# Kernel optimization log

Measured on AMD Instinct MI355X. Metric: run time of the kernel, lower is better.

Reference implementation:

```python
import jax, jax.numpy as jnp
import numpy as np

# physical system constants (from source)
M1, M2 = 1.0, 1.5
K1, K2 = 2.0, 3.0
C1, C2 = 0.5, 0.8
KARNOPP_DV = 0.01
REF_AMP, REF_OMEGA = 0.5, 0.5  # x2_ref_func(t) = 0.5*sin(0.5*t)

N = 1 << 20   # batch of states
H = 64        # friction_nn hidden dim


def setup_inputs() -> dict:
    key = jax.random.key(0)
    ks = jax.random.split(key, 8)
    return {
        "t": jax.random.uniform(ks[0], (N,), dtype=jnp.float32) * 10.0,
        "z": jax.random.normal(ks[1], (5, N), dtype=jnp.float32),
        "logK": jax.random.normal(ks[2], (), dtype=jnp.float32) * 0.1,
        "logz": jax.random.normal(ks[3], (), dtype=jnp.float32) * 0.1 - 0.5,
        "logp": jax.random.normal(ks[4], (), dtype=jnp.float32) * 0.1 + 0.5,
        "W1": jax.random.normal(ks[5], (1, H), dtype=jnp.float32) * 0.5,
        "b1": jnp.zeros((H,), dtype=jnp.float32),
        "W2": jax.random.normal(ks[6], (H, 2), dtype=jnp.float32) * 0.5,
        "b2": jnp.zeros((2,), dtype=jnp.float32),
    }


def _friction_nn(v2, W1, b1, W2, b2):
    # tiny MLP: 1 -> H -> 2, softplus heads for positive magnitudes
    h = jnp.tanh(v2[:, None] * W1[0] + b1)          # [N, H]
    out = h @ W2 + b2                                # [N, 2]
    kinetic_mag = jax.nn.softplus(out[:, 0])
    stiction_limit = jax.nn.softplus(out[:, 1])
    return kinetic_mag, stiction_limit


def reference(t, z, logK, logz, logp, W1, b1, W2, b2):
    x1, v1, x2, v2, xc = z
    K = jnp.exp(logK)
    z_ctrl = jnp.exp(logz)
    p_ctrl = jnp.exp(logp)

    x2_ref = REF_AMP * jnp.sin(REF_OMEGA * t)
    e = x2_ref - x2
    d_xc = -p_ctrl * xc + e
    u = K * (z_ctrl - p_ctrl) * xc + K * e

    dx1_dt = v1
    dv1_dt = (u - K1 * x1 - C1 * v1 - K2 * (x1 - x2) - C2 * (v1 - v2)) / M1
    dx2_dt = v2

    F_net = K2 * (x1 - x2) + C2 * (v1 - v2)
    kinetic_mag, stiction_limit = _friction_nn(v2, W1, b1, W2, b2)
    is_static = jnp.abs(v2) < KARNOPP_DV
    F_static = -jnp.clip(F_net, -stiction_limit, stiction_limit)
    F_kinetic = -kinetic_mag * jnp.sign(v2)
    F_friction = jnp.where(is_static, F_static, F_kinetic)
    dv2_dt = (F_net + F_friction) / M2

    return jnp.stack([dx1_dt, dv1_dt, dx2_dt, dv2_dt, d_xc])  # [5, N]
```

## Files before the change

kernel.cpp:

```cpp
#include <hip/hip_runtime.h>
#include <hip/hip_bf16.h>

#define M1_C 1.0f
#define M2_INV (1.0f / 1.5f)
#define K1_C 2.0f
#define K2_C 3.0f
#define C1_C 0.5f
#define C2_C 0.8f
#define KARNOPP_DV 0.01f
#define REF_AMP 0.5f
#define REF_OMEGA 0.5f
#define HDIM 64

#define LOG2E 1.4426950408889634f
#define LN2 0.6931471805599453f

__device__ __forceinline__ float tanh_fast(float x) {
    float e = __builtin_amdgcn_exp2f(x * (2.0f * LOG2E));
    float r = __builtin_amdgcn_rcpf(e + 1.0f);
    return fmaf(-2.0f, r, 1.0f);
}

__device__ __forceinline__ float softplus_fast(float x) {
    float ax = fabsf(x);
    float e = __builtin_amdgcn_exp2f(-ax * LOG2E);
    float l = __builtin_amdgcn_logf(1.0f + e) * LN2;
    return fmaxf(x, 0.0f) + l;
}

__global__ __launch_bounds__(256) void controlled_system_kernel(
    const float* __restrict__ t,
    const float* __restrict__ z,
    const float* __restrict__ logK,
    const float* __restrict__ logz,
    const float* __restrict__ logp,
    const float* __restrict__ W1,
    const float* __restrict__ b1,
    const float* __restrict__ W2,
    const float* __restrict__ b2,
    float* __restrict__ out,
    int N)
{
    __shared__ float4 wpack[HDIM];
    __shared__ float sb2[2];

    int tid = threadIdx.x;
    if (tid < HDIM) {
        wpack[tid] = make_float4(W1[tid], b1[tid], W2[2 * tid], W2[2 * tid + 1]);
    }
    if (tid < 2) sb2[tid] = b2[tid];
    __syncthreads();

    int i = blockIdx.x * blockDim.x + tid;
    if (i >= N) return;

    float K  = __builtin_amdgcn_exp2f(logK[0] * LOG2E);
    float zc = __builtin_amdgcn_exp2f(logz[0] * LOG2E);
    float pc = __builtin_amdgcn_exp2f(logp[0] * LOG2E);

    float tt = t[i];
    float x1 = z[i];
    float v1 = z[N + i];
    float x2 = z[2 * N + i];
    float v2 = z[3 * N + i];
    float xc = z[4 * N + i];

    float x2_ref = REF_AMP * __sinf(REF_OMEGA * tt);
    float e_ctl = x2_ref - x2;
    float d_xc = fmaf(-pc, xc, e_ctl);
    float u = K * (zc - pc) * xc + K * e_ctl;

    float dx12 = x1 - x2;
    float dv12 = v1 - v2;

    float dv1 = u - K1_C * x1 - C1_C * v1 - K2_C * dx12 - C2_C * dv12;

    float F_net = fmaf(K2_C, dx12, C2_C * dv12);

    float a0 = sb2[0];
    float a1 = sb2[1];
#pragma unroll
    for (int j = 0; j < HDIM; ++j) {
        float4 w = wpack[j];
        float h = tanh_fast(fmaf(v2, w.x, w.y));
        a0 = fmaf(h, w.z, a0);
        a1 = fmaf(h, w.w, a1);
    }
    float kinetic_mag    = softplus_fast(a0);
    float stiction_limit = softplus_fast(a1);

    bool is_static = fabsf(v2) < KARNOPP_DV;
    float F_static = -fminf(fmaxf(F_net, -stiction_limit), stiction_limit);
    float F_kinetic = (v2 > 0.0f) ? -kinetic_mag : kinetic_mag;
    float F_friction = is_static ? F_static : F_kinetic;
    float dv2 = (F_net + F_friction) * M2_INV;

    out[i]         = v1;
    out[N + i]     = dv1;
    out[2 * N + i] = v2;
    out[3 * N + i] = dv2;
    out[4 * N + i] = d_xc;
}

extern "C" void kernel_launch(void* const* d_in, const int* in_sizes, int n_in,
                              void* d_out, int out_size, void* d_ws, size_t ws_size,
                              hipStream_t stream) {
    const float* t    = (const float*)d_in[0];
    const float* z    = (const float*)d_in[1];
    const float* logK = (const float*)d_in[2];
    const float* logz = (const float*)d_in[3];
    const float* logp = (const float*)d_in[4];
    const float* W1   = (const float*)d_in[5];
    const float* b1   = (const float*)d_in[6];
    const float* W2   = (const float*)d_in[7];
    const float* b2   = (const float*)d_in[8];
    float* out = (float*)d_out;

    int N = in_sizes[0];
    int blocks = (N + 255) / 256;
    controlled_system_kernel<<<blocks, 256, 0, stream>>>(
        t, z, logK, logz, logp, W1, b1, W2, b2, out, N);
}
```

Baseline: 103.0 us.

## Process four elements per thread with vectorized IO and shared weight reads

Each thread now computes four consecutive states. It uses float4 loads and stores, and every LDS weight fetch in the 64-wide MLP loop serves all four elements. This reduces LDS traffic and per-thread overhead and increases instruction-level parallelism across the transcendental chains. In exchange it launches fewer threads, uses more registers, and assumes N is a multiple of four with aligned pointers.

```diff
diff --git a/kernel.cpp b/kernel.cpp
--- a/kernel.cpp
+++ b/kernel.cpp
@@ -1,7 +1,7 @@
 #include <hip/hip_runtime.h>
 #include <hip/hip_bf16.h>
 
-#define M1_C 1.0f
+
 #define M2_INV (1.0f / 1.5f)
 #define K1_C 2.0f
 #define K2_C 3.0f
@@ -11,6 +11,8 @@
 #define REF_AMP 0.5f
 #define REF_OMEGA 0.5f
 #define HDIM 64
+#define EPT 4
+#define BLOCK 256
 
 #define LOG2E 1.4426950408889634f
 #define LN2 0.6931471805599453f
@@ -28,7 +30,7 @@
     return fmaxf(x, 0.0f) + l;
 }
 
-__global__ __launch_bounds__(256) void controlled_system_kernel(
+__global__ __launch_bounds__(BLOCK) void controlled_system_kernel(
     const float* __restrict__ t,
     const float* __restrict__ z,
     const float* __restrict__ logK,
@@ -51,55 +53,71 @@
     if (tid < 2) sb2[tid] = b2[tid];
     __syncthreads();
 
-    int i = blockIdx.x * blockDim.x + tid;
-    if (i >= N) return;
+    int i0 = (blockIdx.x * BLOCK + tid) * EPT;
+    if (i0 >= N) return;
 
     float K  = __builtin_amdgcn_exp2f(logK[0] * LOG2E);
     float zc = __builtin_amdgcn_exp2f(logz[0] * LOG2E);
     float pc = __builtin_amdgcn_exp2f(logp[0] * LOG2E);
 
-    float tt = t[i];
-    float x1 = z[i];
-    float v1 = z[N + i];
-    float x2 = z[2 * N + i];
-    float v2 = z[3 * N + i];
-    float xc = z[4 * N + i];
+    float4 t4  = *(const float4*)(t + i0);
+    float4 x1v = *(const float4*)(z + i0);
+    float4 v1v = *(const float4*)(z + N + i0);
+    float4 x2v = *(const float4*)(z + 2 * N + i0);
+    float4 v2v = *(const float4*)(z + 3 * N + i0);
+    float4 xcv = *(const float4*)(z + 4 * N + i0);
 
-    float x2_ref = REF_AMP * __sinf(REF_OMEGA * tt);
-    float e_ctl = x2_ref - x2;
-    float d_xc = fmaf(-pc, xc, e_ctl);
-    float u = K * (zc - pc) * xc + K * e_ctl;
+    float tt[EPT] = {t4.x, t4.y, t4.z, t4.w};
+    float x1[EPT] = {x1v.x, x1v.y, x1v.z, x1v.w};
+    float v1[EPT] = {v1v.x, v1v.y, v1v.z, v1v.w};
+    float x2[EPT] = {x2v.x, x2v.y, x2v.z, x2v.w};
+    float v2[EPT] = {v2v.x, v2v.y, v2v.z, v2v.w};
+    float xc[EPT] = {xcv.x, xcv.y, xcv.z, xcv.w};
 
-    float dx12 = x1 - x2;
-    float dv12 = v1 - v2;
+    float a0[EPT], a1[EPT];
+    float bb0 = sb2[0], bb1 = sb2[1];
+#pragma unroll
+    for (int e = 0; e < EPT; ++e) { a0[e] = bb0; a1[e] = bb1; }
 
-    float dv1 = u - K1_C * x1 - C1_C * v1 - K2_C * dx12 - C2_C * dv12;
-
-    float F_net = fmaf(K2_C, dx12, C2_C * dv12);
-
-    float a0 = sb2[0];
-    float a1 = sb2[1];
-#pragma unroll
+#pragma unroll 4
     for (int j = 0; j < HDIM; ++j) {
         float4 w = wpack[j];
-        float h = tanh_fast(fmaf(v2, w.x, w.y));
-        a0 = fmaf(h, w.z, a0);
-        a1 = fmaf(h, w.w, a1);
+#pragma unroll
+        for (int e = 0; e < EPT; ++e) {
+            float h = tanh_fast(fmaf(v2[e], w.x, w.y));
+            a0[e] = fmaf(h, w.z, a0[e]);
+            a1[e] = fmaf(h, w.w, a1[e]);
+        }
     }
-    float kinetic_mag    = softplus_fast(a0);
-    float stiction_limit = softplus_fast(a1);
 
-    bool is_static = fabsf(v2) < KARNOPP_DV;
-    float F_static = -fminf(fmaxf(F_net, -stiction_limit), stiction_limit);
-    float F_kinetic = (v2 > 0.0f) ? -kinetic_mag : kinetic_mag;
-    float F_friction = is_static ? F_static : F_kinetic;
-    float dv2 = (F_net + F_friction) * M2_INV;
+    float dv1o[EPT], dv2o[EPT], dxco[EPT];
+#pragma unroll
+    for (int e = 0; e < EPT; ++e) {
+        float x2_ref = REF_AMP * __sinf(REF_OMEGA * tt[e]);
+        float e_ctl = x2_ref - x2[e];
+        dxco[e] = fmaf(-pc, xc[e], e_ctl);
+        float u = K * (zc - pc) * xc[e] + K * e_ctl;
 
-    out[i]         = v1;
-    out[N + i]     = dv1;
-    out[2 * N + i] = v2;
-    out[3 * N + i] = dv2;
-    out[4 * N + i] = d_xc;
+        float dx12 = x1[e] - x2[e];
+        float dv12 = v1[e] - v2[e];
+        dv1o[e] = u - K1_C * x1[e] - C1_C * v1[e] - K2_C * dx12 - C2_C * dv12;
+
+        float F_net = fmaf(K2_C, dx12, C2_C * dv12);
+        float kinetic_mag    = softplus_fast(a0[e]);
+        float stiction_limit = softplus_fast(a1[e]);
+
+        bool is_static = fabsf(v2[e]) < KARNOPP_DV;
+        float F_static = -fminf(fmaxf(F_net, -stiction_limit), stiction_limit);
+        float F_kinetic = (v2[e] > 0.0f) ? -kinetic_mag : kinetic_mag;
+        float F_friction = is_static ? F_static : F_kinetic;
+        dv2o[e] = (F_net + F_friction) * M2_INV;
+    }
+
+    *(float4*)(out + i0)         = v1v;
+    *(float4*)(out + N + i0)     = make_float4(dv1o[0], dv1o[1], dv1o[2], dv1o[3]);
+    *(float4*)(out + 2 * N + i0) = v2v;
+    *(float4*)(out + 3 * N + i0) = make_float4(dv2o[0], dv2o[1], dv2o[2], dv2o[3]);
+    *(float4*)(out + 4 * N + i0) = make_float4(dxco[0], dxco[1], dxco[2], dxco[3]);
 }
 
 extern "C" void kernel_launch(void* const* d_in, const int* in_sizes, int n_in,
@@ -117,7 +135,7 @@
     float* out = (float*)d_out;
 
     int N = in_sizes[0];
-    int blocks = (N + 255) / 256;
-    controlled_system_kernel<<<blocks, 256, 0, stream>>>(
+    int blocks = (N + BLOCK * EPT - 1) / (BLOCK * EPT);
+    controlled_system_kernel<<<blocks, BLOCK, 0, stream>>>(
         t, z, logK, logz, logp, W1, b1, W2, b2, out, N);
 }
```

Result: no change. 104.4 us (+1.3%).
